# Kernel optimization log

Measured on AMD Instinct MI355X. Metric: run time of the kernel, lower is better.

Reference implementation:

```python
import jax, jax.numpy as jnp
import numpy as np

N_NODES = 10000
N_EDGES = 320000
H = 8  # n_heads


def _heads(x, n_heads):
    # [E_or_N, m, 2d+1] -> [E_or_N, H, (m//H)*(2d+1)]  (fiber2head)
    n, m, c = x.shape
    return x.reshape(n, n_heads, (m // n_heads) * c)


def setup_inputs() -> dict:
    key = jax.random.key(0)
    ks = jax.random.split(key, 7)
    return {
        "v0": jax.random.normal(ks[0], (N_EDGES, 64, 1), dtype=jnp.float32),
        "v1": jax.random.normal(ks[1], (N_EDGES, 64, 3), dtype=jnp.float32),
        "k0": jax.random.normal(ks[2], (N_EDGES, 64, 1), dtype=jnp.float32),
        "k1": jax.random.normal(ks[3], (N_EDGES, 64, 3), dtype=jnp.float32),
        "q0": jax.random.normal(ks[4], (N_NODES, 64, 1), dtype=jnp.float32),
        "q1": jax.random.normal(ks[5], (N_NODES, 64, 3), dtype=jnp.float32),
        "dst": jax.random.randint(ks[6], (N_EDGES,), 0, N_NODES, dtype=jnp.int32),
    }


def reference(v0, v1, k0, k1, q0, q1, dst):
    # fiber2head: concat per-head-flattened features over degrees
    kh = jnp.concatenate([_heads(k0, H), _heads(k1, H)], axis=-1)  # [E,H,Dh]
    qh = jnp.concatenate([_heads(q0, H), _heads(q1, H)], axis=-1)  # [N,H,Dh]

    d_key = q0.shape[1] * q0.shape[2] + q1.shape[1] * q1.shape[2]  # f_key.n_features = 256

    # e_dot_v('k','q'): edge key . dst-node query, per head
    e = jnp.einsum('ehd,ehd->eh', kh, qh[dst]) / jnp.sqrt(jnp.float32(d_key))  # [E,H]

    # edge_softmax over incoming edges of each destination node
    emax = jax.ops.segment_max(e, dst, num_segments=N_NODES)  # [N,H]
    ex = jnp.exp(e - emax[dst])
    denom = jax.ops.segment_sum(ex, dst, num_segments=N_NODES)  # [N,H]
    a = ex / denom[dst]  # [E,H]

    def agg(v):
        E, m, c = v.shape
        vh = v.reshape(E, H, m // H, c)                      # [E,H,m/H,2d+1]
        msg = a[:, :, None, None] * vh                        # attn-weighted message
        out = jax.ops.segment_sum(msg, dst, num_segments=N_NODES)
        return out.reshape(N_NODES, m, c)                     # [N,m,2d+1]

    return agg(v0), agg(v1)
```

## Files before the change

### kernel.cpp

```cpp
#include <hip/hip_runtime.h>

#define NHEAD 8

__global__ __launch_bounds__(256) void edge_logits_kernel(
    const float* __restrict__ k0, const float* __restrict__ k1,
    const float* __restrict__ q0, const float* __restrict__ q1,
    const int* __restrict__ dst,
    float* __restrict__ exw,
    float* __restrict__ denom,
    int* __restrict__ cnt,
    int E)
{
    const int wid  = threadIdx.x >> 6;
    const int lane = threadIdx.x & 63;
    const int e = blockIdx.x * 4 + wid;
    if (e >= E) return;
    const int n = dst[e];

    const float kv0 = k0[e * 64 + lane];
    const float qv0 = q0[n * 64 + lane];
    const float3 kv1 = *(const float3*)(k1 + (size_t)e * 192 + lane * 3);
    const float3 qv1 = *(const float3*)(q1 + (size_t)n * 192 + lane * 3);

    float p = kv0 * qv0 + kv1.x * qv1.x + kv1.y * qv1.y + kv1.z * qv1.z;
    p += __shfl_xor(p, 1);
    p += __shfl_xor(p, 2);
    p += __shfl_xor(p, 4);

    if ((lane & 7) == 0) {
        const float ex = __expf(p * 0.0625f);
        const int h = lane >> 3;
        exw[e * NHEAD + h] = ex;
        atomicAdd(&denom[n * NHEAD + h], ex);
    }
    if (lane == 0) atomicAdd(&cnt[n], 1);
}

__global__ __launch_bounds__(1024) void scan_kernel(
    const int* __restrict__ cnt, int* __restrict__ offs,
    int* __restrict__ cursor, int n)
{
    __shared__ int sdata[1024];
    const int tid = threadIdx.x;
    const int items = (n + 1023) >> 10;
    const int base = tid * items;
    int local[16];
    int sum = 0;
    for (int i = 0; i < items && i < 16; ++i) {
        int idx = base + i;
        int v = (idx < n) ? cnt[idx] : 0;
        local[i] = sum;
        sum += v;
    }
    sdata[tid] = sum;
    __syncthreads();
    for (int off = 1; off < 1024; off <<= 1) {
        int v = (tid >= off) ? sdata[tid - off] : 0;
        __syncthreads();
        sdata[tid] += v;
        __syncthreads();
    }
    const int prev = (tid > 0) ? sdata[tid - 1] : 0;
    for (int i = 0; i < items && i < 16; ++i) {
        int idx = base + i;
        if (idx < n) {
            int o = prev + local[i];
            offs[idx] = o;
            cursor[idx] = o;
        }
    }
    if (tid == 0) offs[n] = sdata[1023];
}

__global__ __launch_bounds__(256) void scatter_kernel(
    const int* __restrict__ dst, int* __restrict__ cursor,
    int* __restrict__ eids, int E)
{
    const int e = blockIdx.x * 256 + threadIdx.x;
    if (e >= E) return;
    const int n = dst[e];
    const int p = atomicAdd(&cursor[n], 1);
    eids[p] = e;
}

__global__ __launch_bounds__(256) void agg_kernel(
    const float* __restrict__ v0, const float* __restrict__ v1,
    const float* __restrict__ exw, const float* __restrict__ denom,
    const int* __restrict__ offs, const int* __restrict__ eids,
    float* __restrict__ out, int N)
{
    __shared__ int se[256];
    const int n = blockIdx.x;
    const int t = threadIdx.x;
    const int h = (t < 64) ? (t >> 3) : ((t - 64) / 24);

    const int start = offs[n];
    const int end   = offs[n + 1];

    float acc = 0.f;
    for (int base = start; base < end; base += 256) {
        const int c = min(256, end - base);
        __syncthreads();
        if (t < c) se[t] = eids[base + t];
        __syncthreads();
        for (int i = 0; i < c; ++i) {
            const int e = se[i];
            const float w = exw[e * NHEAD + h];
            const float v = (t < 64) ? v0[e * 64 + t]
                                     : v1[(size_t)e * 192 + (t - 64)];
            acc += w * v;
        }
    }
    const float d = denom[n * NHEAD + h];
    const float invd = (end > start) ? (1.0f / d) : 0.0f;
    acc *= invd;

    if (t < 64) out[n * 64 + t] = acc;
    else        out[(size_t)N * 64 + (size_t)n * 192 + (t - 64)] = acc;
}

extern "C" void kernel_launch(void* const* d_in, const int* in_sizes, int n_in,
                              void* d_out, int out_size, void* d_ws, size_t ws_size,
                              hipStream_t stream) {
    const float* v0 = (const float*)d_in[0];
    const float* v1 = (const float*)d_in[1];
    const float* k0 = (const float*)d_in[2];
    const float* k1 = (const float*)d_in[3];
    const float* q0 = (const float*)d_in[4];
    const float* q1 = (const float*)d_in[5];
    const int*  dst = (const int*)d_in[6];

    const int E = in_sizes[6];
    const int N = in_sizes[4] / 64;

    char* ws = (char*)d_ws;
    size_t off = 0;
    float* exw = (float*)(ws + off);   off += (size_t)E * NHEAD * 4;
    float* denom = (float*)(ws + off); off += (size_t)N * NHEAD * 4;
    int* cnt = (int*)(ws + off);       off += (size_t)N * 4;
    size_t zero_from = (char*)denom - ws;
    size_t zero_len  = off - zero_from;
    int* offs = (int*)(ws + off);      off += (size_t)(N + 1) * 4;
    off = (off + 15) & ~(size_t)15;
    int* cursor = (int*)(ws + off);    off += (size_t)N * 4;
    off = (off + 15) & ~(size_t)15;
    int* eids = (int*)(ws + off);      off += (size_t)E * 4;

    hipMemsetAsync(ws + zero_from, 0, zero_len, stream);

    edge_logits_kernel<<<(E + 3) / 4, 256, 0, stream>>>(
        k0, k1, q0, q1, dst, exw, denom, cnt, E);

    scan_kernel<<<1, 1024, 0, stream>>>(cnt, offs, cursor, N);

    scatter_kernel<<<(E + 255) / 256, 256, 0, stream>>>(dst, cursor, eids, E);

    agg_kernel<<<N, 256, 0, stream>>>(
        v0, v1, exw, denom, offs, eids, (float*)d_out, N);
}
```

Before: 621.8 us.

## Fuse edge scatter into logits kernel and vectorize aggregation with float4 loads

Adds a separate count kernel so the CSR offsets exist before the edge pass. The edge-logit kernel can then also scatter edge ids, removing the standalone scatter kernel and a read of dst. The edge kernel remaps lanes so each loads a float4 covering one head's slice. The aggregation kernel shrinks to one 64-thread wavefront per node, with each thread accumulating a float4. Edge ids are broadcast via shuffles instead of shared memory, and value reads use nontemporal loads. Fewer threads per node may reduce memory-level parallelism in the gather-heavy aggregation.

```diff
diff --git a/kernel.cpp b/kernel.cpp
--- a/kernel.cpp
+++ b/kernel.cpp
@@ -1,39 +1,13 @@
 #include <hip/hip_runtime.h>
 
 #define NHEAD 8
+typedef float f4 __attribute__((ext_vector_type(4)));
 
-__global__ __launch_bounds__(256) void edge_logits_kernel(
-    const float* __restrict__ k0, const float* __restrict__ k1,
-    const float* __restrict__ q0, const float* __restrict__ q1,
-    const int* __restrict__ dst,
-    float* __restrict__ exw,
-    float* __restrict__ denom,
-    int* __restrict__ cnt,
-    int E)
+__global__ __launch_bounds__(256) void count_kernel(
+    const int* __restrict__ dst, int* __restrict__ cnt, int E)
 {
-    const int wid  = threadIdx.x >> 6;
-    const int lane = threadIdx.x & 63;
-    const int e = blockIdx.x * 4 + wid;
-    if (e >= E) return;
-    const int n = dst[e];
-
-    const float kv0 = k0[e * 64 + lane];
-    const float qv0 = q0[n * 64 + lane];
-    const float3 kv1 = *(const float3*)(k1 + (size_t)e * 192 + lane * 3);
-    const float3 qv1 = *(const float3*)(q1 + (size_t)n * 192 + lane * 3);
-
-    float p = kv0 * qv0 + kv1.x * qv1.x + kv1.y * qv1.y + kv1.z * qv1.z;
-    p += __shfl_xor(p, 1);
-    p += __shfl_xor(p, 2);
-    p += __shfl_xor(p, 4);
-
-    if ((lane & 7) == 0) {
-        const float ex = __expf(p * 0.0625f);
-        const int h = lane >> 3;
-        exw[e * NHEAD + h] = ex;
-        atomicAdd(&denom[n * NHEAD + h], ex);
-    }
-    if (lane == 0) atomicAdd(&cnt[n], 1);
+    const int i = blockIdx.x * 256 + threadIdx.x;
+    if (i < E) atomicAdd(&cnt[dst[i]], 1);
 }
 
 __global__ __launch_bounds__(1024) void scan_kernel(
@@ -72,42 +46,77 @@
     if (tid == 0) offs[n] = sdata[1023];
 }
 
-__global__ __launch_bounds__(256) void scatter_kernel(
-    const int* __restrict__ dst, int* __restrict__ cursor,
-    int* __restrict__ eids, int E)
+__global__ __launch_bounds__(256) void edge_kernel(
+    const float* __restrict__ k0, const float* __restrict__ k1,
+    const float* __restrict__ q0, const float* __restrict__ q1,
+    const int* __restrict__ dst,
+    float* __restrict__ exw,
+    float* __restrict__ denom,
+    int* __restrict__ cursor,
+    int* __restrict__ eids,
+    int E)
 {
-    const int e = blockIdx.x * 256 + threadIdx.x;
+    const int wid  = threadIdx.x >> 6;
+    const int lane = threadIdx.x & 63;
+    const int e = blockIdx.x * 4 + wid;
     if (e >= E) return;
     const int n = dst[e];
-    const int p = atomicAdd(&cursor[n], 1);
-    eids[p] = e;
+    const int h = lane >> 3;
+    const int j = lane & 7;
+
+    const float* kp;
+    const float* qp;
+    if (j < 6) {
+        kp = k1 + (size_t)e * 192 + h * 24 + j * 4;
+        qp = q1 + (size_t)n * 192 + h * 24 + j * 4;
+    } else {
+        kp = k0 + (size_t)e * 64 + h * 8 + (j - 6) * 4;
+        qp = q0 + (size_t)n * 64 + h * 8 + (j - 6) * 4;
+    }
+    const f4 kv = __builtin_nontemporal_load((const f4*)kp);
+    const f4 qv = *(const f4*)qp;
+
+    float p = kv.x * qv.x + kv.y * qv.y + kv.z * qv.z + kv.w * qv.w;
+    p += __shfl_xor(p, 1);
+    p += __shfl_xor(p, 2);
+    p += __shfl_xor(p, 4);
+
+    if (j == 0) {
+        const float ex = __expf(p * 0.0625f);
+        exw[e * NHEAD + h] = ex;
+        atomicAdd(&denom[n * NHEAD + h], ex);
+    }
+    if (lane == 0) {
+        const int p0 = atomicAdd(&cursor[n], 1);
+        eids[p0] = e;
+    }
 }
 
-__global__ __launch_bounds__(256) void agg_kernel(
+__global__ __launch_bounds__(64) void agg_kernel(
     const float* __restrict__ v0, const float* __restrict__ v1,
     const float* __restrict__ exw, const float* __restrict__ denom,
     const int* __restrict__ offs, const int* __restrict__ eids,
     float* __restrict__ out, int N)
 {
-    __shared__ int se[256];
     const int n = blockIdx.x;
     const int t = threadIdx.x;
-    const int h = (t < 64) ? (t >> 3) : ((t - 64) / 24);
+    const int h = (t < 16) ? (t >> 1) : ((4 * (t - 16)) / 24);
+    const float* vb = (t < 16) ? (v0 + t * 4) : (v1 + (size_t)(t - 16) * 4);
+    const int vstride = (t < 16) ? 64 : 192;
 
     const int start = offs[n];
     const int end   = offs[n + 1];
 
-    float acc = 0.f;
-    for (int base = start; base < end; base += 256) {
-        const int c = min(256, end - base);
-        __syncthreads();
-        if (t < c) se[t] = eids[base + t];
-        __syncthreads();
+    f4 acc = {0.f, 0.f, 0.f, 0.f};
+    for (int base = start; base < end; base += 64) {
+        const int c = min(64, end - base);
+        const int eid = (base + t < end) ? eids[base + t] : 0;
+        #pragma unroll 4
         for (int i = 0; i < c; ++i) {
-            const int e = se[i];
+            const int e = __shfl(eid, i);
             const float w = exw[e * NHEAD + h];
-            const float v = (t < 64) ? v0[e * 64 + t]
-                                     : v1[(size_t)e * 192 + (t - 64)];
+            const f4 v = __builtin_nontemporal_load(
+                (const f4*)(vb + (size_t)e * vstride));
             acc += w * v;
         }
     }
@@ -115,8 +124,8 @@
     const float invd = (end > start) ? (1.0f / d) : 0.0f;
     acc *= invd;
 
-    if (t < 64) out[n * 64 + t] = acc;
-    else        out[(size_t)N * 64 + (size_t)n * 192 + (t - 64)] = acc;
+    if (t < 16) *(f4*)(out + (size_t)n * 64 + t * 4) = acc;
+    else        *(f4*)(out + (size_t)N * 64 + (size_t)n * 192 + (t - 16) * 4) = acc;
 }
 
 extern "C" void kernel_launch(void* const* d_in, const int* in_sizes, int n_in,
@@ -148,13 +157,13 @@
 
     hipMemsetAsync(ws + zero_from, 0, zero_len, stream);
 
-    edge_logits_kernel<<<(E + 3) / 4, 256, 0, stream>>>(
-        k0, k1, q0, q1, dst, exw, denom, cnt, E);
+    count_kernel<<<(E + 255) / 256, 256, 0, stream>>>(dst, cnt, E);
 
     scan_kernel<<<1, 1024, 0, stream>>>(cnt, offs, cursor, N);
 
-    scatter_kernel<<<(E + 255) / 256, 256, 0, stream>>>(dst, cursor, eids, E);
+    edge_kernel<<<(E + 3) / 4, 256, 0, stream>>>(
+        k0, k1, q0, q1, dst, exw, denom, cursor, eids, E);
 
-    agg_kernel<<<N, 256, 0, stream>>>(
+    agg_kernel<<<N, 64, 0, stream>>>(
         v0, v1, exw, denom, offs, eids, (float*)d_out, N);
 }
```

Result: slower. 651.4 us (+4.8%).
